# Kernel optimization log

Hardware: AMD Instinct MI355X
Metric: run time of the kernel (lower is better)

Reference implementation:

```python
import jax, jax.numpy as jnp
import numpy as np

D_MODEL = 1024
N_HEADS = 16
TOP_FACTOR = 5


def setup_inputs() -> dict:
    key = jax.random.key(0)
    ks = jax.random.split(key, 9)
    B, L, D = 2, 4096, D_MODEL
    s = 0.02
    return {
        "x": jax.random.normal(ks[0], (B, L, D), dtype=jnp.float32),
        "Wq": jax.random.normal(ks[1], (D, D), dtype=jnp.float32) * s,
        "bq": jnp.zeros((D,), dtype=jnp.float32),
        "Wk": jax.random.normal(ks[2], (D, D), dtype=jnp.float32) * s,
        "bk": jnp.zeros((D,), dtype=jnp.float32),
        "Wv": jax.random.normal(ks[3], (D, D), dtype=jnp.float32) * s,
        "bv": jnp.zeros((D,), dtype=jnp.float32),
        "Wo": jax.random.normal(ks[4], (D, D), dtype=jnp.float32) * s,
        "bo": jnp.zeros((D,), dtype=jnp.float32),
    }


def reference(x, Wq, bq, Wk, bk, Wv, bv, Wo, bo):
    B, L, D = x.shape
    H = N_HEADS
    hd = D // H
    BH = B * H
    top_u = max(1, L // TOP_FACTOR)

    def proj(W, b):
        # [B,L,D] -> [B*H, L, hd] (matches view + transpose(1,2) in torch)
        y = x @ W.T + b
        return y.reshape(B, L, H, hd).transpose(0, 2, 1, 3).reshape(BH, L, hd)

    Q = proj(Wq, bq)
    K = proj(Wk, bk)
    V = proj(Wv, bv)

    # select top-u queries per (batch,head) by L2 norm
    query_norms = jnp.linalg.norm(Q, axis=2)              # [BH, L]
    _, top_idx = jax.lax.top_k(query_norms, top_u)        # [BH, top_u]
    Q_sel = jnp.take_along_axis(Q, top_idx[:, :, None], axis=1)  # [BH, u, hd]

    scale = 1.0 / (hd ** 0.5)
    scores = jnp.einsum('bud,bld->bul', Q_sel, K) * scale  # [BH, u, L]
    attn = jax.nn.softmax(scores, axis=-1)
    out_sel = jnp.einsum('bul,bld->bud', attn, V)          # [BH, u, hd]

    # scatter selected outputs back; non-selected rows stay zero
    out_full = jnp.zeros((BH, L, hd), dtype=x.dtype)
    out_full = out_full.at[jnp.arange(BH)[:, None], top_idx].set(out_sel)

    out = out_full.reshape(B, H, L, hd).transpose(0, 2, 1, 3).reshape(B, L, D)
    return out @ Wo.T + bo
```

## Files before the change

kernel.cpp:

```cpp
#include <hip/hip_runtime.h>
#include <cstddef>
#include <cstdint>

constexpr int LSEQ = 4096;
constexpr int DM   = 1024;
constexpr int HD   = 64;
constexpr int BHT  = 32;
constexpr int TOPU = 819;
constexpr int MROWS = 8192;

typedef unsigned short u16;
typedef __attribute__((ext_vector_type(8))) short short8v;
typedef __attribute__((ext_vector_type(4))) short short4v;
typedef __attribute__((ext_vector_type(4))) float f32x4;

__device__ __forceinline__ u16 f2bf(float f) {
  uint32_t u = __float_as_uint(f);
  u += 0x7fffu + ((u >> 16) & 1u);
  return (u16)(u >> 16);
}
__device__ __forceinline__ float bf2f(u16 h) {
  return __uint_as_float(((uint32_t)h) << 16);
}

__device__ __forceinline__ void gl16(const void* g, void* l) {
  __builtin_amdgcn_global_load_lds(
      (const __attribute__((address_space(1))) void*)g,
      (__attribute__((address_space(3))) void*)l, 16, 0, 0);
}

__device__ __forceinline__ void inv_swz(int S, int& R, int& C) {
  const int R0 = ((S >> 5) ^ (S >> 7)) & 1;
  const int R1 = (S >> 6) & 1;
  R = ((S >> 6) << 1) | R0;
  C = (((S >> 3) & 1) ^ R0) | ((((S >> 4) & 1) ^ R1) << 1);
}

__global__ __launch_bounds__(256) void split3_kernel(
    const float* __restrict__ src, u16* __restrict__ p1,
    u16* __restrict__ p2, u16* __restrict__ p3, int n8)
{
  int i = blockIdx.x * 256 + threadIdx.x;
  if (i >= n8) return;
  const float4 a = *reinterpret_cast<const float4*>(src + (size_t)i * 8);
  const float4 b = *reinterpret_cast<const float4*>(src + (size_t)i * 8 + 4);
  float e[8] = {a.x, a.y, a.z, a.w, b.x, b.y, b.z, b.w};
  short8v v1, v2, v3;
  #pragma unroll
  for (int j = 0; j < 8; ++j) {
    u16 h1 = f2bf(e[j]);        float r1 = e[j] - bf2f(h1);
    u16 h2 = f2bf(r1);          float r2 = r1 - bf2f(h2);
    u16 h3 = f2bf(r2);
    v1[j] = (short)h1; v2[j] = (short)h2; v3[j] = (short)h3;
  }
  *reinterpret_cast<short8v*>(p1 + (size_t)i * 8) = v1;
  *reinterpret_cast<short8v*>(p2 + (size_t)i * 8) = v2;
  *reinterpret_cast<short8v*>(p3 + (size_t)i * 8) = v3;
}

__global__ __launch_bounds__(256) void conv_bf16(
    const float* __restrict__ src, u16* __restrict__ dst, int n8)
{
  int i = blockIdx.x * 256 + threadIdx.x;
  if (i >= n8) return;
  const float4 a = *reinterpret_cast<const float4*>(src + (size_t)i * 8);
  const float4 b = *reinterpret_cast<const float4*>(src + (size_t)i * 8 + 4);
  short8v v;
  v[0] = (short)f2bf(a.x); v[1] = (short)f2bf(a.y);
  v[2] = (short)f2bf(a.z); v[3] = (short)f2bf(a.w);
  v[4] = (short)f2bf(b.x); v[5] = (short)f2bf(b.y);
  v[6] = (short)f2bf(b.z); v[7] = (short)f2bf(b.w);
  *reinterpret_cast<short8v*>(dst + (size_t)i * 8) = v;
}

__global__ __launch_bounds__(256) void gemm_q_split(
    const u16* __restrict__ X1, const u16* __restrict__ X2, const u16* __restrict__ X3,
    const u16* __restrict__ W1, const u16* __restrict__ W2, const u16* __restrict__ W3,
    const float* __restrict__ bias, float* __restrict__ Y)
{
  __shared__ u16 As[3][128 * 32];
  __shared__ u16 Bs[3][128 * 32];
  const int tid = threadIdx.x;
  const int m0 = blockIdx.x * 128, n0 = blockIdx.y * 128;
  const int wid = tid >> 6, lane = tid & 63;
  const int wr = (wid >> 1) * 64, wc = (wid & 1) * 64;
  const int c = lane & 15, G = lane >> 4;

  int Rr[2], Cr[2];
  #pragma unroll
  for (int rr = 0; rr < 2; ++rr) inv_swz((tid + rr * 256) * 8, Rr[rr], Cr[rr]);

  f32x4 acc[4][4];
  #pragma unroll
  for (int mt = 0; mt < 4; ++mt)
    #pragma unroll
    for (int nt = 0; nt < 4; ++nt)
      acc[mt][nt] = (f32x4){0.f, 0.f, 0.f, 0.f};

  for (int k0 = 0; k0 < DM; k0 += 32) {
    #pragma unroll
    for (int rr = 0; rr < 2; ++rr) {
      const size_t goA = (size_t)(m0 + Rr[rr]) * DM + k0 + Cr[rr] * 8;
      const size_t goB = (size_t)(n0 + Rr[rr]) * DM + k0 + Cr[rr] * 8;
      const int lb = wid * 512 + rr * 2048;
      gl16(X1 + goA, &As[0][lb]);
      gl16(X2 + goA, &As[1][lb]);
      gl16(X3 + goA, &As[2][lb]);
      gl16(W1 + goB, &Bs[0][lb]);
      gl16(W2 + goB, &Bs[1][lb]);
      gl16(W3 + goB, &Bs[2][lb]);
    }
    __syncthreads();

    short8v bf[3][4];
    #pragma unroll
    for (int nt = 0; nt < 4; ++nt) {
      const int n = wc + nt * 16 + c;
      const int eo = (n * 32 + G * 8) ^ ((n & 7) << 3);
      bf[0][nt] = *reinterpret_cast<const short8v*>(&Bs[0][eo]);
      bf[1][nt] = *reinterpret_cast<const short8v*>(&Bs[1][eo]);
      bf[2][nt] = *reinterpret_cast<const short8v*>(&Bs[2][eo]);
    }
    #pragma unroll
    for (int mt = 0; mt < 4; ++mt) {
      const int m = wr + mt * 16 + c;
      const int eo = (m * 32 + G * 8) ^ ((m & 7) << 3);
      short8v a1 = *reinterpret_cast<const short8v*>(&As[0][eo]);
      short8v a2 = *reinterpret_cast<const short8v*>(&As[1][eo]);
      short8v a3 = *reinterpret_cast<const short8v*>(&As[2][eo]);
      #pragma unroll
      for (int nt = 0; nt < 4; ++nt) {
        acc[mt][nt] = __builtin_amdgcn_mfma_f32_16x16x32_bf16(a1, bf[0][nt], acc[mt][nt], 0, 0, 0);
        acc[mt][nt] = __builtin_amdgcn_mfma_f32_16x16x32_bf16(a1, bf[1][nt], acc[mt][nt], 0, 0, 0);
        acc[mt][nt] = __builtin_amdgcn_mfma_f32_16x16x32_bf16(a2, bf[0][nt], acc[mt][nt], 0, 0, 0);
        acc[mt][nt] = __builtin_amdgcn_mfma_f32_16x16x32_bf16(a2, bf[1][nt], acc[mt][nt], 0, 0, 0);
        acc[mt][nt] = __builtin_amdgcn_mfma_f32_16x16x32_bf16(a1, bf[2][nt], acc[mt][nt], 0, 0, 0);
        acc[mt][nt] = __builtin_amdgcn_mfma_f32_16x16x32_bf16(a3, bf[0][nt], acc[mt][nt], 0, 0, 0);
      }
    }
    __syncthreads();
  }

  float bb[4];
  #pragma unroll
  for (int nt = 0; nt < 4; ++nt) bb[nt] = bias[n0 + wc + nt * 16 + c];

  #pragma unroll
  for (int mt = 0; mt < 4; ++mt) {
    #pragma unroll
    for (int nt = 0; nt < 4; ++nt) {
      const int n = n0 + wc + nt * 16 + c;
      const int h = n >> 6, d = n & 63;
      #pragma unroll
      for (int r = 0; r < 4; ++r) {
        const int m = m0 + wr + mt * 16 + G * 4 + r;
        const int b = m >> 12, l = m & (LSEQ - 1);
        Y[((size_t)((b << 4) + h) * LSEQ + l) * HD + d] = acc[mt][nt][r] + bb[nt];
      }
    }
  }
}

template<int MODE>
__global__ __launch_bounds__(256) void gemm_bf16(
    const u16* __restrict__ Xb, const u16* __restrict__ Wb,
    const float* __restrict__ bias, void* __restrict__ Yout)
{
  __shared__ u16 As[128 * 32];
  __shared__ u16 Bs[128 * 32];
  const int tid = threadIdx.x;
  const int m0 = blockIdx.x * 128, n0 = blockIdx.y * 128;
  const int wid = tid >> 6, lane = tid & 63;
  const int wr = (wid >> 1) * 64, wc = (wid & 1) * 64;
  const int c = lane & 15, G = lane >> 4;

  int Rr[2], Cr[2];
  #pragma unroll
  for (int rr = 0; rr < 2; ++rr) inv_swz((tid + rr * 256) * 8, Rr[rr], Cr[rr]);

  f32x4 acc[4][4];
  #pragma unroll
  for (int mt = 0; mt < 4; ++mt)
    #pragma unroll
    for (int nt = 0; nt < 4; ++nt)
      acc[mt][nt] = (f32x4){0.f, 0.f, 0.f, 0.f};

  for (int k0 = 0; k0 < DM; k0 += 32) {
    #pragma unroll
    for (int rr = 0; rr < 2; ++rr) {
      const size_t goA = (size_t)(m0 + Rr[rr]) * DM + k0 + Cr[rr] * 8;
      const size_t goB = (size_t)(n0 + Rr[rr]) * DM + k0 + Cr[rr] * 8;
      const int lb = wid * 512 + rr * 2048;
      gl16(Xb + goA, As + lb);
      gl16(Wb + goB, Bs + lb);
    }
    __syncthreads();

    short8v af[4], bf[4];
    #pragma unroll
    for (int mt = 0; mt < 4; ++mt) {
      const int m = wr + mt * 16 + c;
      af[mt] = *reinterpret_cast<const short8v*>(As + ((m * 32 + G * 8) ^ ((m & 7) << 3)));
      const int n = wc + mt * 16 + c;
      bf[mt] = *reinterpret_cast<const short8v*>(Bs + ((n * 32 + G * 8) ^ ((n & 7) << 3)));
    }
    #pragma unroll
    for (int mt = 0; mt < 4; ++mt)
      #pragma unroll
      for (int nt = 0; nt < 4; ++nt)
        acc[mt][nt] = __builtin_amdgcn_mfma_f32_16x16x32_bf16(af[mt], bf[nt], acc[mt][nt], 0, 0, 0);
    __syncthreads();
  }

  float bb[4];
  #pragma unroll
  for (int nt = 0; nt < 4; ++nt) bb[nt] = bias[n0 + wc + nt * 16 + c];

  if constexpr (MODE == 2) {
    __shared__ u16 T[128 * 136];
    #pragma unroll
    for (int mt = 0; mt < 4; ++mt) {
      #pragma unroll
      for (int nt = 0; nt < 4; ++nt) {
        const int n = wc + nt * 16 + c;
        const int mloc = wr + mt * 16 + G * 4;
        short4v pv;
        #pragma unroll
        for (int r = 0; r < 4; ++r) pv[r] = (short)f2bf(acc[mt][nt][r] + bb[nt]);
        *reinterpret_cast<short4v*>(T + n * 136 + mloc) = pv;
      }
    }
    __syncthreads();
    u16* Y = (u16*)Yout;
    const int bb2 = m0 >> 12;
    const int ml0 = m0 & (LSEQ - 1);
    #pragma unroll
    for (int uu = 0; uu < 8; ++uu) {
      const int u = uu * 256 + tid;
      const int n = u >> 4, kg = u & 15;
      short8v vvv = *reinterpret_cast<const short8v*>(T + n * 136 + kg * 8);
      const int h = (n0 + n) >> 6, d = (n0 + n) & 63;
      *reinterpret_cast<short8v*>(
          Y + ((size_t)((bb2 << 4) + h) * HD + d) * LSEQ + ml0 + kg * 8) = vvv;
    }
  } else {
    #pragma unroll
    for (int mt = 0; mt < 4; ++mt) {
      #pragma unroll
      for (int nt = 0; nt < 4; ++nt) {
        const int n = n0 + wc + nt * 16 + c;
        #pragma unroll
        for (int r = 0; r < 4; ++r) {
          const int m = m0 + wr + mt * 16 + G * 4 + r;
          const float val = acc[mt][nt][r] + bb[nt];
          if (MODE == 0) {
            const int b = m >> 12, l = m & (LSEQ - 1), h = n >> 6, d = n & 63;
            u16* Y = (u16*)Yout;
            Y[((size_t)((b << 4) + h) * LSEQ + l) * HD + d] = f2bf(val);
          } else {
            float* Y = (float*)Yout;
            Y[(size_t)m * DM + n] = val;
          }
        }
      }
    }
  }
}

__global__ __launch_bounds__(256) void norms_kernel(
    const float* __restrict__ Q, float* __restrict__ norms)
{
  const int r = blockIdx.x * 256 + threadIdx.x;
  const float4* row = reinterpret_cast<const float4*>(Q + (size_t)r * HD);
  float s = 0.f;
  #pragma unroll
  for (int i = 0; i < 16; ++i) {
    float4 v = row[i];
    s += v.x * v.x + v.y * v.y + v.z * v.z + v.w * v.w;
  }
  norms[r] = s;
}

__global__ __launch_bounds__(1024) void select_topk(
    const float* __restrict__ norms, int* __restrict__ top_idx)
{
  __shared__ unsigned int keys[LSEQ];
  __shared__ unsigned int hist[256];
  __shared__ unsigned int wsums[16];
  __shared__ unsigned int sh_b, sh_above;

  const int tid = threadIdx.x;
  const int bh = blockIdx.x;

  for (int l = tid; l < LSEQ; l += 1024)
    keys[l] = __float_as_uint(norms[bh * LSEQ + l]);
  __syncthreads();

  unsigned int prefix = 0, rem = TOPU, total_gt = 0;
  for (int shift = 24; shift >= 0; shift -= 8) {
    if (tid < 256) hist[tid] = 0;
    __syncthreads();
    for (int l = tid; l < LSEQ; l += 1024) {
      const unsigned int k = keys[l];
      const bool in = (shift == 24) || ((k >> (shift + 8)) == prefix);
      if (in) atomicAdd(&hist[(k >> shift) & 255], 1);
    }
    __syncthreads();
    if (tid == 0) {
      unsigned int cum = 0; int b = 255;
      for (; b > 0; --b) {
        const unsigned int h = hist[b];
        if (cum + h >= rem) break;
        cum += h;
      }
      sh_b = (unsigned int)b; sh_above = cum;
    }
    __syncthreads();
    prefix = (prefix << 8) | sh_b;
    total_gt += sh_above;
    rem -= sh_above;
    __syncthreads();
  }
  const unsigned int T = prefix;

  const int lane = tid & 63, wv = tid >> 6;
  const int l0 = tid * 4;

  {
    unsigned int flags = 0; int cnt = 0;
    #pragma unroll
    for (int j = 0; j < 4; ++j)
      if (keys[l0 + j] > T) { flags |= 1u << j; ++cnt; }
    int incl = cnt;
    #pragma unroll
    for (int off = 1; off < 64; off <<= 1) {
      int nv = __shfl_up(incl, off);
      if (lane >= off) incl += nv;
    }
    if (lane == 63) wsums[wv] = (unsigned int)incl;
    __syncthreads();
    if (tid == 0) {
      unsigned int run = 0;
      for (int w = 0; w < 16; ++w) { unsigned int t = wsums[w]; wsums[w] = run; run += t; }
    }
    __syncthreads();
    unsigned int pos = wsums[wv] + (unsigned int)(incl - cnt);
    #pragma unroll
    for (int j = 0; j < 4; ++j)
      if (flags & (1u << j)) top_idx[bh * TOPU + (pos++)] = l0 + j;
  }
  __syncthreads();

  {
    unsigned int flags = 0; int cnt = 0;
    #pragma unroll
    for (int j = 0; j < 4; ++j)
      if (keys[l0 + j] == T) { flags |= 1u << j; ++cnt; }
    int incl = cnt;
    #pragma unroll
    for (int off = 1; off < 64; off <<= 1) {
      int nv = __shfl_up(incl, off);
      if (lane >= off) incl += nv;
    }
    if (lane == 63) wsums[wv] = (unsigned int)incl;
    __syncthreads();
    if (tid == 0) {
      unsigned int run = 0;
      for (int w = 0; w < 16; ++w) { unsigned int t = wsums[w]; wsums[w] = run; run += t; }
    }
    __syncthreads();
    unsigned int r0 = wsums[wv] + (unsigned int)(incl - cnt);
    #pragma unroll
    for (int j = 0; j < 4; ++j)
      if (flags & (1u << j)) {
        if (r0 < rem) top_idx[bh * TOPU + total_gt + r0] = l0 + j;
        ++r0;
      }
  }
}

__global__ __launch_bounds__(256) void attn_mfma(
    const float* __restrict__ Qf, const u16* __restrict__ Kg,
    const u16* __restrict__ VgT, const int* __restrict__ tix,
    float* __restrict__ Opart, float* __restrict__ MLpart)
{
  __shared__ u16 Kc[128 * 64];
  __shared__ u16 Vt[64 * 128];
  __shared__ u16 Pt[4][16 * 136];

  const int tid = threadIdx.x;
  const int wid = tid >> 6, lane = tid & 63;
  const int c = lane & 15, G = lane >> 4;

  const int l = blockIdx.x;
  const int grp = l >> 3;
  const int bh = (grp / 26) * 8 + (l & 7);
  const int rem = grp % 26;
  const int qb = rem >> 1, ks = rem & 1;

  const size_t bhL = (size_t)bh * LSEQ;
  const int rglob = qb * 64 + wid * 16 + c;
  const int rowidx = (rglob < TOPU) ? tix[bh * TOPU + rglob] : -1;

  short8v qf[2];
  #pragma unroll
  for (int kf = 0; kf < 2; ++kf) {
    if (rowidx >= 0) {
      const float* qp = Qf + (bhL + rowidx) * HD + kf * 32 + G * 8;
      const float4 x0 = *reinterpret_cast<const float4*>(qp);
      const float4 x1 = *reinterpret_cast<const float4*>(qp + 4);
      short8v v;
      v[0] = (short)f2bf(x0.x * 0.125f); v[1] = (short)f2bf(x0.y * 0.125f);
      v[2] = (short)f2bf(x0.z * 0.125f); v[3] = (short)f2bf(x0.w * 0.125f);
      v[4] = (short)f2bf(x1.x * 0.125f); v[5] = (short)f2bf(x1.y * 0.125f);
      v[6] = (short)f2bf(x1.z * 0.125f); v[7] = (short)f2bf(x1.w * 0.125f);
      qf[kf] = v;
    } else {
      short8v v;
      #pragma unroll
      for (int j = 0; j < 8; ++j) v[j] = 0;
      qf[kf] = v;
    }
  }

  float m = -1e30f, lsum = 0.f;
  f32x4 oacc[4];
  #pragma unroll
  for (int dt = 0; dt < 4; ++dt) oacc[dt] = (f32x4){0.f, 0.f, 0.f, 0.f};

  const int ko0 = ks * (LSEQ / 2);
  for (int t = 0; t < LSEQ / 256; ++t) {
    const int ko = ko0 + t * 128;
    #pragma unroll
    for (int uu = 0; uu < 4; ++uu) {
      const int u = uu * 256 + tid;
      const int key = u >> 3, dg = u & 7;
      short8v kv = *reinterpret_cast<const short8v*>(
          Kg + (bhL + ko + key) * HD + dg * 8);
      *reinterpret_cast<short8v*>(Kc + key * 64 + ((dg ^ (key & 7)) << 3)) = kv;
      const int d = u >> 4, kg = u & 15;
      short8v vv = *reinterpret_cast<const short8v*>(
          VgT + ((size_t)bh * HD + d) * LSEQ + ko + kg * 8);
      *reinterpret_cast<short8v*>(Vt + d * 128 + ((kg ^ (d & 7)) << 3)) = vv;
    }
    __syncthreads();

    f32x4 sacc[8];
    __builtin_amdgcn_s_setprio(1);
    #pragma unroll
    for (int kt = 0; kt < 8; ++kt) {
      const int key = kt * 16 + c;
      short8v kb0 = *reinterpret_cast<const short8v*>(
          Kc + key * 64 + (((0 + G) ^ (key & 7)) << 3));
      short8v kb1 = *reinterpret_cast<const short8v*>(
          Kc + key * 64 + (((4 + G) ^ (key & 7)) << 3));
      f32x4 s = (f32x4){0.f, 0.f, 0.f, 0.f};
      s = __builtin_amdgcn_mfma_f32_16x16x32_bf16(kb0, qf[0], s, 0, 0, 0);
      s = __builtin_amdgcn_mfma_f32_16x16x32_bf16(kb1, qf[1], s, 0, 0, 0);
      sacc[kt] = s;
    }
    __builtin_amdgcn_s_setprio(0);

    float smax = -1e30f;
    #pragma unroll
    for (int kt = 0; kt < 8; ++kt) {
      float a0 = fmaxf(sacc[kt][0], sacc[kt][1]);
      float a1 = fmaxf(sacc[kt][2], sacc[kt][3]);
      smax = fmaxf(smax, fmaxf(a0, a1));
    }
    smax = fmaxf(smax, __shfl_xor(smax, 16));
    smax = fmaxf(smax, __shfl_xor(smax, 32));
    const float mnew = fmaxf(m, smax);
    const float corr = __expf(m - mnew);
    float ssum = 0.f;
    #pragma unroll
    for (int kt = 0; kt < 8; ++kt) {
      float p0 = __expf(sacc[kt][0] - mnew);
      float p1 = __expf(sacc[kt][1] - mnew);
      float p2 = __expf(sacc[kt][2] - mnew);
      float p3 = __expf(sacc[kt][3] - mnew);
      ssum += (p0 + p1) + (p2 + p3);
      short4v pv;
      pv[0] = (short)f2bf(p0); pv[1] = (short)f2bf(p1);
      pv[2] = (short)f2bf(p2); pv[3] = (short)f2bf(p3);
      *reinterpret_cast<short4v*>(&Pt[wid][c * 136 + kt * 16 + G * 4]) = pv;
    }
    ssum += __shfl_xor(ssum, 16);
    ssum += __shfl_xor(ssum, 32);
    lsum = lsum * corr + ssum;
    m = mnew;
    #pragma unroll
    for (int dt = 0; dt < 4; ++dt) oacc[dt] *= corr;

    __builtin_amdgcn_s_setprio(1);
    #pragma unroll
    for (int kf = 0; kf < 4; ++kf) {
      short8v pf = *reinterpret_cast<const short8v*>(
          &Pt[wid][c * 136 + kf * 32 + G * 8]);
      #pragma unroll
      for (int dt = 0; dt < 4; ++dt) {
        const int d = dt * 16 + c;
        short8v vf = *reinterpret_cast<const short8v*>(
            Vt + d * 128 + (((kf * 4 + G) ^ (d & 7)) << 3));
        oacc[dt] = __builtin_amdgcn_mfma_f32_16x16x32_bf16(vf, pf, oacc[dt], 0, 0, 0);
      }
    }
    __builtin_amdgcn_s_setprio(0);
    __syncthreads();
  }

  const int q = wid * 16 + c;
  const size_t pb = ((size_t)(bh * 13 + qb) * 2 + ks) * 64 + q;
  float* op = Opart + pb * 64;
  #pragma unroll
  for (int dt = 0; dt < 4; ++dt)
    *reinterpret_cast<f32x4*>(op + dt * 16 + G * 4) = oacc[dt];
  if (G == 0) {
    MLpart[pb * 2]     = m;
    MLpart[pb * 2 + 1] = lsum;
  }
}

__global__ __launch_bounds__(256) void attn_combine(
    const float* __restrict__ Opart, const float* __restrict__ MLpart,
    const int* __restrict__ tix, u16* __restrict__ O1b)
{
  const int bq = blockIdx.x;
  const int bh = bq / 13, qb = bq % 13;
  const int tid = threadIdx.x;
  const int q = tid >> 2, dq = (tid & 3) * 16;
  const int rglob = qb * 64 + q;
  if (rglob >= TOPU) return;
  const int rowidx = tix[bh * TOPU + rglob];

  const size_t p0 = ((size_t)bq * 2 + 0) * 64 + q;
  const size_t p1 = ((size_t)bq * 2 + 1) * 64 + q;
  const float m0 = MLpart[p0 * 2], l0 = MLpart[p0 * 2 + 1];
  const float m1 = MLpart[p1 * 2], l1 = MLpart[p1 * 2 + 1];
  const float mx = fmaxf(m0, m1);
  const float c0 = __expf(m0 - mx), c1 = __expf(m1 - mx);
  const float linv = 1.0f / (l0 * c0 + l1 * c1);

  const int b = bh >> 4, h = bh & 15;
  u16* dst = O1b + (size_t)(b * LSEQ + rowidx) * DM + h * HD + dq;
  const float* o0 = Opart + p0 * 64 + dq;
  const float* o1 = Opart + p1 * 64 + dq;
  #pragma unroll
  for (int i = 0; i < 16; i += 4) {
    float4 a  = *reinterpret_cast<const float4*>(o0 + i);
    float4 bb = *reinterpret_cast<const float4*>(o1 + i);
    short4v o;
    o[0] = (short)f2bf((a.x * c0 + bb.x * c1) * linv);
    o[1] = (short)f2bf((a.y * c0 + bb.y * c1) * linv);
    o[2] = (short)f2bf((a.z * c0 + bb.z * c1) * linv);
    o[3] = (short)f2bf((a.w * c0 + bb.w * c1) * linv);
    *reinterpret_cast<short4v*>(dst + i) = o;
  }
}

extern "C" void kernel_launch(void* const* d_in, const int* in_sizes, int n_in,
                              void* d_out, int out_size, void* d_ws, size_t ws_size,
                              hipStream_t stream) {
  const float* x  = (const float*)d_in[0];
  const float* Wq = (const float*)d_in[1];
  const float* bq = (const float*)d_in[2];
  const float* Wk = (const float*)d_in[3];
  const float* bk = (const float*)d_in[4];
  const float* Wv = (const float*)d_in[5];
  const float* bv = (const float*)d_in[6];
  const float* Wo = (const float*)d_in[7];
  const float* bo = (const float*)d_in[8];
  float* out = (float*)d_out;

  char* w = (char*)d_ws;
  float* Qb = (float*)w;  w += (size_t)BHT * LSEQ * HD * 4;
  u16* x1   = (u16*)w;    w += (size_t)MROWS * DM * 2;
  u16* x2   = (u16*)w;    w += (size_t)MROWS * DM * 2;
  u16* x3   = (u16*)w;    w += (size_t)MROWS * DM * 2;
  u16* VgT  = (u16*)w;    w += (size_t)BHT * HD * LSEQ * 2;
  u16* Wkb  = (u16*)w;    w += (size_t)DM * DM * 2;
  u16* Wvb  = (u16*)w;    w += (size_t)DM * DM * 2;
  u16* Wob  = (u16*)w;    w += (size_t)DM * DM * 2;
  u16* wq1  = (u16*)w;    w += (size_t)DM * DM * 2;
  u16* wq2  = (u16*)w;    w += (size_t)DM * DM * 2;
  u16* wq3  = (u16*)w;    w += (size_t)DM * DM * 2;

  u16*   O1b   = x2;
  u16*   Kb    = x3;
  float* norms = (float*)wq1;
  int*   tix   = (int*)wq2;
  float* Opart  = (float*)x1;
  float* MLpart = Opart + (size_t)832 * 64 * 64;

  split3_kernel<<<4096, 256, 0, stream>>>(x,  x1,  x2,  x3,  MROWS * DM / 8);
  split3_kernel<<<512,  256, 0, stream>>>(Wq, wq1, wq2, wq3, DM * DM / 8);
  conv_bf16<<<512, 256, 0, stream>>>(Wk, Wkb, DM * DM / 8);
  conv_bf16<<<512, 256, 0, stream>>>(Wv, Wvb, DM * DM / 8);
  conv_bf16<<<512, 256, 0, stream>>>(Wo, Wob, DM * DM / 8);

  gemm_q_split<<<dim3(MROWS / 128, DM / 128), 256, 0, stream>>>(
      x1, x2, x3, wq1, wq2, wq3, bq, Qb);

  gemm_bf16<0><<<dim3(MROWS / 128, DM / 128), 256, 0, stream>>>(x1, Wkb, bk, (void*)Kb);
  gemm_bf16<2><<<dim3(MROWS / 128, DM / 128), 256, 0, stream>>>(x1, Wvb, bv, (void*)VgT);

  norms_kernel<<<BHT * LSEQ / 256, 256, 0, stream>>>(Qb, norms);
  select_topk<<<BHT, 1024, 0, stream>>>(norms, tix);

  hipMemsetAsync(O1b, 0, (size_t)MROWS * DM * 2, stream);

  attn_mfma<<<832, 256, 0, stream>>>(Qb, Kb, VgT, tix, Opart, MLpart);
  attn_combine<<<416, 256, 0, stream>>>(Opart, MLpart, tix, O1b);

  gemm_bf16<1><<<dim3(MROWS / 128, DM / 128), 256, 0, stream>>>(O1b, Wob, bo, (void*)out);
}
```

Measured before the change: 319.8 us.

## Fuse prep kernels, fold Q norms into Q GEMM, merge K/V GEMMs

```diff
diff --git a/kernel.cpp b/kernel.cpp
--- a/kernel.cpp
+++ b/kernel.cpp
@@ -36,12 +36,8 @@
   C = (((S >> 3) & 1) ^ R0) | ((((S >> 4) & 1) ^ R1) << 1);
 }
 
-__global__ __launch_bounds__(256) void split3_kernel(
-    const float* __restrict__ src, u16* __restrict__ p1,
-    u16* __restrict__ p2, u16* __restrict__ p3, int n8)
-{
-  int i = blockIdx.x * 256 + threadIdx.x;
-  if (i >= n8) return;
+__device__ __forceinline__ void split3_body(const float* src, u16* p1, u16* p2,
+                                            u16* p3, int i) {
   const float4 a = *reinterpret_cast<const float4*>(src + (size_t)i * 8);
   const float4 b = *reinterpret_cast<const float4*>(src + (size_t)i * 8 + 4);
   float e[8] = {a.x, a.y, a.z, a.w, b.x, b.y, b.z, b.w};
@@ -58,11 +54,7 @@
   *reinterpret_cast<short8v*>(p3 + (size_t)i * 8) = v3;
 }
 
-__global__ __launch_bounds__(256) void conv_bf16(
-    const float* __restrict__ src, u16* __restrict__ dst, int n8)
-{
-  int i = blockIdx.x * 256 + threadIdx.x;
-  if (i >= n8) return;
+__device__ __forceinline__ void conv_body(const float* src, u16* dst, int i) {
   const float4 a = *reinterpret_cast<const float4*>(src + (size_t)i * 8);
   const float4 b = *reinterpret_cast<const float4*>(src + (size_t)i * 8 + 4);
   short8v v;
@@ -73,10 +65,33 @@
   *reinterpret_cast<short8v*>(dst + (size_t)i * 8) = v;
 }
 
+__global__ __launch_bounds__(256) void prep_all(
+    const float* __restrict__ x,  const float* __restrict__ Wq,
+    const float* __restrict__ Wk, const float* __restrict__ Wv,
+    const float* __restrict__ Wo,
+    u16* __restrict__ x1, u16* __restrict__ x2, u16* __restrict__ x3,
+    u16* __restrict__ wq1, u16* __restrict__ wq2, u16* __restrict__ wq3,
+    u16* __restrict__ Wkb, u16* __restrict__ Wvb, u16* __restrict__ Wob)
+{
+  const int NX = MROWS * DM / 8;
+  const int NW = DM * DM / 8;
+  int i = blockIdx.x * 256 + threadIdx.x;
+  if (i < NX)                { split3_body(x,  x1,  x2,  x3,  i); return; }
+  i -= NX;
+  if (i < NW)                { split3_body(Wq, wq1, wq2, wq3, i); return; }
+  i -= NW;
+  if (i < NW)                { conv_body(Wk, Wkb, i); return; }
+  i -= NW;
+  if (i < NW)                { conv_body(Wv, Wvb, i); return; }
+  i -= NW;
+  if (i < NW)                { conv_body(Wo, Wob, i); }
+}
+
 __global__ __launch_bounds__(256) void gemm_q_split(
     const u16* __restrict__ X1, const u16* __restrict__ X2, const u16* __restrict__ X3,
     const u16* __restrict__ W1, const u16* __restrict__ W2, const u16* __restrict__ W3,
-    const float* __restrict__ bias, float* __restrict__ Y)
+    const float* __restrict__ bias, float* __restrict__ Y,
+    float* __restrict__ norms)
 {
   __shared__ u16 As[3][128 * 32];
   __shared__ u16 Bs[3][128 * 32];
@@ -145,6 +160,12 @@
   #pragma unroll
   for (int nt = 0; nt < 4; ++nt) bb[nt] = bias[n0 + wc + nt * 16 + c];
 
+  float ns[4][4];
+  #pragma unroll
+  for (int mt = 0; mt < 4; ++mt)
+    #pragma unroll
+    for (int r = 0; r < 4; ++r) ns[mt][r] = 0.f;
+
   #pragma unroll
   for (int mt = 0; mt < 4; ++mt) {
     #pragma unroll
@@ -155,16 +176,139 @@
       for (int r = 0; r < 4; ++r) {
         const int m = m0 + wr + mt * 16 + G * 4 + r;
         const int b = m >> 12, l = m & (LSEQ - 1);
-        Y[((size_t)((b << 4) + h) * LSEQ + l) * HD + d] = acc[mt][nt][r] + bb[nt];
-      }
-    }
-  }
-}
-
-template<int MODE>
-__global__ __launch_bounds__(256) void gemm_bf16(
+        const float val = acc[mt][nt][r] + bb[nt];
+        Y[((size_t)((b << 4) + h) * LSEQ + l) * HD + d] = val;
+        ns[mt][r] = fmaf(val, val, ns[mt][r]);
+      }
+    }
+  }
+  #pragma unroll
+  for (int mt = 0; mt < 4; ++mt)
+    #pragma unroll
+    for (int r = 0; r < 4; ++r) {
+      float v = ns[mt][r];
+      v += __shfl_xor(v, 1); v += __shfl_xor(v, 2);
+      v += __shfl_xor(v, 4); v += __shfl_xor(v, 8);
+      ns[mt][r] = v;
+    }
+  if (c == 0) {
+    const int h = (n0 + wc) >> 6;
+    #pragma unroll
+    for (int mt = 0; mt < 4; ++mt)
+      #pragma unroll
+      for (int r = 0; r < 4; ++r) {
+        const int m = m0 + wr + mt * 16 + G * 4 + r;
+        const int b = m >> 12, l = m & (LSEQ - 1);
+        norms[(((size_t)((b << 4) + h)) << 12) + l] = ns[mt][r];
+      }
+  }
+}
+
+__global__ __launch_bounds__(256) void gemm_kv(
+    const u16* __restrict__ Xb, const u16* __restrict__ Wkb, const u16* __restrict__ Wvb,
+    const float* __restrict__ bkp, const float* __restrict__ bvp,
+    u16* __restrict__ Kb, u16* __restrict__ VgT)
+{
+  __shared__ u16 smem[128 * 136];
+  u16* As = smem;
+  u16* Bs = smem + 4096;
+  const int tid = threadIdx.x;
+  const bool isV = blockIdx.y >= 8;
+  const int m0 = blockIdx.x * 128, n0 = (blockIdx.y & 7) * 128;
+  const u16* Wb = isV ? Wvb : Wkb;
+  const float* bias = isV ? bvp : bkp;
+  const int wid = tid >> 6, lane = tid & 63;
+  const int wr = (wid >> 1) * 64, wc = (wid & 1) * 64;
+  const int c = lane & 15, G = lane >> 4;
+
+  int Rr[2], Cr[2];
+  #pragma unroll
+  for (int rr = 0; rr < 2; ++rr) inv_swz((tid + rr * 256) * 8, Rr[rr], Cr[rr]);
+
+  f32x4 acc[4][4];
+  #pragma unroll
+  for (int mt = 0; mt < 4; ++mt)
+    #pragma unroll
+    for (int nt = 0; nt < 4; ++nt)
+      acc[mt][nt] = (f32x4){0.f, 0.f, 0.f, 0.f};
+
+  for (int k0 = 0; k0 < DM; k0 += 32) {
+    #pragma unroll
+    for (int rr = 0; rr < 2; ++rr) {
+      const size_t goA = (size_t)(m0 + Rr[rr]) * DM + k0 + Cr[rr] * 8;
+      const size_t goB = (size_t)(n0 + Rr[rr]) * DM + k0 + Cr[rr] * 8;
+      const int lb = wid * 512 + rr * 2048;
+      gl16(Xb + goA, As + lb);
+      gl16(Wb + goB, Bs + lb);
+    }
+    __syncthreads();
+
+    short8v af[4], bf[4];
+    #pragma unroll
+    for (int mt = 0; mt < 4; ++mt) {
+      const int m = wr + mt * 16 + c;
+      af[mt] = *reinterpret_cast<const short8v*>(As + ((m * 32 + G * 8) ^ ((m & 7) << 3)));
+      const int n = wc + mt * 16 + c;
+      bf[mt] = *reinterpret_cast<const short8v*>(Bs + ((n * 32 + G * 8) ^ ((n & 7) << 3)));
+    }
+    #pragma unroll
+    for (int mt = 0; mt < 4; ++mt)
+      #pragma unroll
+      for (int nt = 0; nt < 4; ++nt)
+        acc[mt][nt] = __builtin_amdgcn_mfma_f32_16x16x32_bf16(af[mt], bf[nt], acc[mt][nt], 0, 0, 0);
+    __syncthreads();
+  }
+
+  float bb[4];
+  #pragma unroll
+  for (int nt = 0; nt < 4; ++nt) bb[nt] = bias[n0 + wc + nt * 16 + c];
+
+  if (isV) {
+    #pragma unroll
+    for (int mt = 0; mt < 4; ++mt) {
+      #pragma unroll
+      for (int nt = 0; nt < 4; ++nt) {
+        const int n = wc + nt * 16 + c;
+        const int mloc = wr + mt * 16 + G * 4;
+        short4v pv;
+        #pragma unroll
+        for (int r = 0; r < 4; ++r) pv[r] = (short)f2bf(acc[mt][nt][r] + bb[nt]);
+        *reinterpret_cast<short4v*>(smem + n * 136 + mloc) = pv;
+      }
+    }
+    __syncthreads();
+    const int bb2 = m0 >> 12;
+    const int ml0 = m0 & (LSEQ - 1);
+    #pragma unroll
+    for (int uu = 0; uu < 8; ++uu) {
+      const int u = uu * 256 + tid;
+      const int n = u >> 4, kg = u & 15;
+      short8v vvv = *reinterpret_cast<const short8v*>(smem + n * 136 + kg * 8);
+      const int h = (n0 + n) >> 6, d = (n0 + n) & 63;
+      *reinterpret_cast<short8v*>(
+          VgT + ((size_t)((bb2 << 4) + h) * HD + d) * LSEQ + ml0 + kg * 8) = vvv;
+    }
+  } else {
+    #pragma unroll
+    for (int mt = 0; mt < 4; ++mt) {
+      #pragma unroll
+      for (int nt = 0; nt < 4; ++nt) {
+        const int n = n0 + wc + nt * 16 + c;
+        const int h = n >> 6, d = n & 63;
+        #pragma unroll
+        for (int r = 0; r < 4; ++r) {
+          const int m = m0 + wr + mt * 16 + G * 4 + r;
+          const int b = m >> 12, l = m & (LSEQ - 1);
+          Kb[((size_t)((b << 4) + h) * LSEQ + l) * HD + d] = f2bf(acc[mt][nt][r] + bb[nt]);
+        }
+      }
+    }
+  }
+}
+
+__global__ __launch_bounds__(256) void gemm_out(
     const u16* __restrict__ Xb, const u16* __restrict__ Wb,
-    const float* __restrict__ bias, void* __restrict__ Yout)
+    const float* __restrict__ bias, float* __restrict__ Y)
 {
   __shared__ u16 As[128 * 32];
   __shared__ u16 Bs[128 * 32];
@@ -216,69 +360,18 @@
   #pragma unroll
   for (int nt = 0; nt < 4; ++nt) bb[nt] = bias[n0 + wc + nt * 16 + c];
 
-  if constexpr (MODE == 2) {
-    __shared__ u16 T[128 * 136];
-    #pragma unroll
-    for (int mt = 0; mt < 4; ++mt) {
-      #pragma unroll
-      for (int nt = 0; nt < 4; ++nt) {
-        const int n = wc + nt * 16 + c;
-        const int mloc = wr + mt * 16 + G * 4;
-        short4v pv;
-        #pragma unroll
-        for (int r = 0; r < 4; ++r) pv[r] = (short)f2bf(acc[mt][nt][r] + bb[nt]);
-        *reinterpret_cast<short4v*>(T + n * 136 + mloc) = pv;
-      }
-    }
-    __syncthreads();
-    u16* Y = (u16*)Yout;
-    const int bb2 = m0 >> 12;
-    const int ml0 = m0 & (LSEQ - 1);
-    #pragma unroll
-    for (int uu = 0; uu < 8; ++uu) {
-      const int u = uu * 256 + tid;
-      const int n = u >> 4, kg = u & 15;
-      short8v vvv = *reinterpret_cast<const short8v*>(T + n * 136 + kg * 8);
-      const int h = (n0 + n) >> 6, d = (n0 + n) & 63;
-      *reinterpret_cast<short8v*>(
-          Y + ((size_t)((bb2 << 4) + h) * HD + d) * LSEQ + ml0 + kg * 8) = vvv;
-    }
-  } else {
-    #pragma unroll
-    for (int mt = 0; mt < 4; ++mt) {
-      #pragma unroll
-      for (int nt = 0; nt < 4; ++nt) {
-        const int n = n0 + wc + nt * 16 + c;
-        #pragma unroll
-        for (int r = 0; r < 4; ++r) {
-          const int m = m0 + wr + mt * 16 + G * 4 + r;
-          const float val = acc[mt][nt][r] + bb[nt];
-          if (MODE == 0) {
-            const int b = m >> 12, l = m & (LSEQ - 1), h = n >> 6, d = n & 63;
-            u16* Y = (u16*)Yout;
-            Y[((size_t)((b << 4) + h) * LSEQ + l) * HD + d] = f2bf(val);
-          } else {
-            float* Y = (float*)Yout;
-            Y[(size_t)m * DM + n] = val;
-          }
-        }
-      }
-    }
-  }
-}
-
-__global__ __launch_bounds__(256) void norms_kernel(
-    const float* __restrict__ Q, float* __restrict__ norms)
-{
-  const int r = blockIdx.x * 256 + threadIdx.x;
-  const float4* row = reinterpret_cast<const float4*>(Q + (size_t)r * HD);
-  float s = 0.f;
-  #pragma unroll
-  for (int i = 0; i < 16; ++i) {
-    float4 v = row[i];
-    s += v.x * v.x + v.y * v.y + v.z * v.z + v.w * v.w;
-  }
-  norms[r] = s;
+  #pragma unroll
+  for (int mt = 0; mt < 4; ++mt) {
+    #pragma unroll
+    for (int nt = 0; nt < 4; ++nt) {
+      const int n = n0 + wc + nt * 16 + c;
+      #pragma unroll
+      for (int r = 0; r < 4; ++r) {
+        const int m = m0 + wr + mt * 16 + G * 4 + r;
+        Y[(size_t)m * DM + n] = acc[mt][nt][r] + bb[nt];
+      }
+    }
+  }
 }
 
 __global__ __launch_bounds__(1024) void select_topk(
@@ -429,19 +522,16 @@
   for (int dt = 0; dt < 4; ++dt) oacc[dt] = (f32x4){0.f, 0.f, 0.f, 0.f};
 
   const int ko0 = ks * (LSEQ / 2);
+  const int wbase = (tid & ~63) * 8;
   for (int t = 0; t < LSEQ / 256; ++t) {
     const int ko = ko0 + t * 128;
     #pragma unroll
     for (int uu = 0; uu < 4; ++uu) {
-      const int u = uu * 256 + tid;
-      const int key = u >> 3, dg = u & 7;
-      short8v kv = *reinterpret_cast<const short8v*>(
-          Kg + (bhL + ko + key) * HD + dg * 8);
-      *reinterpret_cast<short8v*>(Kc + key * 64 + ((dg ^ (key & 7)) << 3)) = kv;
-      const int d = u >> 4, kg = u & 15;
-      short8v vv = *reinterpret_cast<const short8v*>(
-          VgT + ((size_t)bh * HD + d) * LSEQ + ko + kg * 8);
-      *reinterpret_cast<short8v*>(Vt + d * 128 + ((kg ^ (d & 7)) << 3)) = vv;
+      const int S = (uu * 256 + tid) * 8;
+      const int key = S >> 6, dgk = ((S >> 3) & 7) ^ (key & 7);
+      gl16(Kg + (bhL + ko + key) * HD + dgk * 8, Kc + uu * 2048 + wbase);
+      const int d = S >> 7, kgv = ((S >> 3) & 15) ^ (d & 7);
+      gl16(VgT + ((size_t)bh * HD + d) * LSEQ + ko + kgv * 8, Vt + uu * 2048 + wbase);
     }
     __syncthreads();
 
@@ -584,27 +674,22 @@
   u16* wq1  = (u16*)w;    w += (size_t)DM * DM * 2;
   u16* wq2  = (u16*)w;    w += (size_t)DM * DM * 2;
   u16* wq3  = (u16*)w;    w += (size_t)DM * DM * 2;
-
-  u16*   O1b   = x2;
-  u16*   Kb    = x3;
-  float* norms = (float*)wq1;
-  int*   tix   = (int*)wq2;
+  float* norms = (float*)w; w += (size_t)BHT * LSEQ * 4;
+
+  u16*   O1b  = x2;
+  u16*   Kb   = x3;
+  int*   tix  = (int*)wq2;
   float* Opart  = (float*)x1;
   float* MLpart = Opart + (size_t)832 * 64 * 64;
 
-  split3_kernel<<<4096, 256, 0, stream>>>(x,  x1,  x2,  x3,  MROWS * DM / 8);
-  split3_kernel<<<512,  256, 0, stream>>>(Wq, wq1, wq2, wq3, DM * DM / 8);
-  conv_bf16<<<512, 256, 0, stream>>>(Wk, Wkb, DM * DM / 8);
-  conv_bf16<<<512, 256, 0, stream>>>(Wv, Wvb, DM * DM / 8);
-  conv_bf16<<<512, 256, 0, stream>>>(Wo, Wob, DM * DM / 8);
+  prep_all<<<6144, 256, 0, stream>>>(x, Wq, Wk, Wv, Wo,
+                                     x1, x2, x3, wq1, wq2, wq3, Wkb, Wvb, Wob);
 
   gemm_q_split<<<dim3(MROWS / 128, DM / 128), 256, 0, stream>>>(
-      x1, x2, x3, wq1, wq2, wq3, bq, Qb);
-
-  gemm_bf16<0><<<dim3(MROWS / 128, DM / 128), 256, 0, stream>>>(x1, Wkb, bk, (void*)Kb);
-  gemm_bf16<2><<<dim3(MROWS / 128, DM / 128), 256, 0, stream>>>(x1, Wvb, bv, (void*)VgT);
-
-  norms_kernel<<<BHT * LSEQ / 256, 256, 0, stream>>>(Qb, norms);
+      x1, x2, x3, wq1, wq2, wq3, bq, Qb, norms);
+
+  gemm_kv<<<dim3(MROWS / 128, 16), 256, 0, stream>>>(x1, Wkb, Wvb, bk, bv, Kb, VgT);
+
   select_topk<<<BHT, 1024, 0, stream>>>(norms, tix);
 
   hipMemsetAsync(O1b, 0, (size_t)MROWS * DM * 2, stream);
@@ -612,5 +697,5 @@
   attn_mfma<<<832, 256, 0, stream>>>(Qb, Kb, VgT, tix, Opart, MLpart);
   attn_combine<<<416, 256, 0, stream>>>(Opart, MLpart, tix, O1b);
 
-  gemm_bf16<1><<<dim3(MROWS / 128, DM / 128), 256, 0, stream>>>(O1b, Wob, bo, (void*)out);
-}
+  gemm_out<<<dim3(MROWS / 128, DM / 128), 256, 0, stream>>>(O1b, Wob, bo, out);
+}
```

Result: faster. 303.5 us (-5.1%).
